# Optimization experiments

Hardware: AMD Instinct MI355X
Metric: run time of the kernel (lower is better)

## Reference

```python
import jax, jax.numpy as jnp
import numpy as np

N_NODES = 20000
N_EDGES = 640000
K_CHEB = 20


def setup_inputs() -> dict:
    key = jax.random.key(0)
    ks = jax.random.split(key, 8)
    x = jax.random.normal(ks[0], (128, N_NODES, 1), dtype=jnp.float32)
    rows = jax.random.randint(ks[1], (N_EDGES,), 0, N_NODES, dtype=jnp.int32)
    cols = jax.random.randint(ks[2], (N_EDGES,), 0, N_NODES, dtype=jnp.int32)
    # rescaled-Laplacian-like values, small scale so the K=20 recursion stays bounded
    vals = jax.random.normal(ks[3], (N_EDGES,), dtype=jnp.float32) * 0.05
    W_gc = jax.random.normal(ks[4], (K_CHEB, 10), dtype=jnp.float32) * 0.1
    b_gc = jnp.zeros((10,), dtype=jnp.float32)
    W_fc = jax.random.normal(ks[5], (N_NODES * 10, 10), dtype=jnp.float32) * 0.01
    b_fc = jnp.zeros((10,), dtype=jnp.float32)
    return {"x": x, "rows": rows, "cols": cols, "vals": vals,
            "W_gc": W_gc, "b_gc": b_gc, "W_fc": W_fc, "b_fc": b_fc}


def reference(x, rows, cols, vals, W_gc, b_gc, W_fc, b_fc):
    B, N, Fin = x.shape  # Fin == 1
    x0 = x[..., 0].T  # [N, B]

    def spmm(t):  # sparse L @ t via edge-list scatter-add, t: [N, B]
        return jax.ops.segment_sum(vals[:, None] * t[cols], rows, num_segments=N)

    # Chebyshev recursion: T0 = x, T1 = L x, Tk = 2 L T_{k-1} - T_{k-2}
    Ts = [x0, spmm(x0)]
    for _ in range(K_CHEB - 2):
        Ts.append(2.0 * spmm(Ts[-1]) - Ts[-2])
    Xt = jnp.stack(Ts, axis=-1)  # [N, B, K]

    gc = jnp.einsum('nbk,kf->bnf', Xt, W_gc) + b_gc  # [B, N, 10]
    gc = jax.nn.relu(gc)
    flat = gc.reshape(B, N * 10)
    h = jax.nn.relu(flat @ W_fc + b_fc)  # [B, 10]
    return jax.nn.softmax(h, axis=1)
```

## Files before the change

### kernel.cpp

```cpp
#include <hip/hip_runtime.h>
#include <hip/hip_bf16.h>
#include <hip/hip_fp16.h>
#include <math.h>


#define NF 10
#define KCHEB 20
#define BCG 64
#define COFF (KCHEB * BCG)

typedef unsigned int u32;


__global__ void init_kernel(int* counts, float* h_part, int N, int H) {
    int i = blockIdx.x * blockDim.x + threadIdx.x;
    if (i < N) counts[i] = 0;
    if (i < H) h_part[i] = 0.f;
}

__global__ void hist_kernel(const int* __restrict__ rows, int* __restrict__ counts, int E) {
    int e = blockIdx.x * blockDim.x + threadIdx.x;
    if (e < E) atomicAdd(&counts[rows[e]], 1);
}

#define SCAN_THREADS 1024
__global__ void scan_kernel(const int* __restrict__ counts, int* __restrict__ row_start,
                            int* __restrict__ cursor, int N) {
    __shared__ int sh[SCAN_THREADS];
    int t = threadIdx.x;
    int CH = (N + SCAN_THREADS - 1) / SCAN_THREADS;
    int base = t * CH;
    int sum = 0;
    for (int i = 0; i < CH; ++i) {
        int idx = base + i;
        sum += (idx < N) ? counts[idx] : 0;
    }
    sh[t] = sum;
    __syncthreads();
    for (int off = 1; off < SCAN_THREADS; off <<= 1) {
        int v = (t >= off) ? sh[t - off] : 0;
        __syncthreads();
        sh[t] += v;
        __syncthreads();
    }
    int run = (t == 0) ? 0 : sh[t - 1];
    for (int i = 0; i < CH; ++i) {
        int idx = base + i;
        if (idx < N) {
            int v = counts[idx];
            row_start[idx] = run;
            cursor[idx] = run;
            run += v;
        }
    }
    if (t == SCAN_THREADS - 1) row_start[N] = run;
}

__global__ void scatter_kernel(const int* __restrict__ rows, const int* __restrict__ cols,
                               const float* __restrict__ vals, int* __restrict__ cursor,
                               int2* __restrict__ csr, int E) {
    int e = blockIdx.x * blockDim.x + threadIdx.x;
    if (e >= E) return;
    int p = atomicAdd(&cursor[rows[e]], 1);
    csr[p] = make_int2(cols[e] * BCG, __float_as_int(vals[e]));
}


__global__ void transpose_kernel(const float* __restrict__ x, float* __restrict__ Xt32,
                                 __half* __restrict__ X16, int N, int ntiles, int b0s) {
    __shared__ float tile[BCG][65];
    int tid = threadIdx.x;
    int g = blockIdx.x / ntiles;
    int ti = blockIdx.x - g * ntiles;
    int n0 = ti * 64;
#pragma unroll
    for (int p = 0; p < 16; ++p) {
        int idx = p * 256 + tid;
        int row = idx >> 6;
        int col = idx & 63;
        if (n0 + col < N)
            tile[row][col] = x[(size_t)(b0s + g * BCG + row) * N + n0 + col];
    }
    __syncthreads();
#pragma unroll
    for (int p = 0; p < 16; ++p) {
        int idx = p * 256 + tid;
        int nloc = idx >> 6;
        int bb = idx & 63;
        int n = n0 + nloc;
        if (n < N) {
            float v = tile[bb][nloc];
            Xt32[((size_t)g * N + n) * COFF + bb] = v;
            X16[((size_t)(g * 2 + 0) * N + n) * BCG + bb] = __float2half_rn(v);
        }
    }
}


__global__ __launch_bounds__(256)
void spmm_kernel(float* __restrict__ Xt32, __half* __restrict__ X16,
                 const int* __restrict__ row_start, const int2* __restrict__ csr,
                 int N, int xpcShift, int subsPerChunk,
                 int ringIn, int ringOut, int kPrev, int kOut,
                 float alpha, float beta) {
    int xcd = blockIdx.x & 7;
    int chunk = xcd >> xpcShift;
    int xpcMask = (1 << xpcShift) - 1;
    int sub = (blockIdx.x >> 3) * (1 << xpcShift) + (xcd & xpcMask);
    if (sub >= subsPerChunk) return;
    int tid = threadIdx.x;
    int ln = tid >> 3;
    int bq = tid & 7;
    int n = sub * 32 + ln;
    if (n >= N) return;
    int s = row_start[n];
    int e = row_start[n + 1];

    const __half* gin = X16 + ((size_t)(chunk * 2 + ringIn) * N) * BCG;
    int bo = bq * 8;
    float acc[8];
#pragma unroll
    for (int q = 0; q < 8; ++q) acc[q] = 0.f;

    int i = s;
    for (; i + 4 <= e; i += 4) {
        int2 p0 = csr[i], p1 = csr[i + 1], p2 = csr[i + 2], p3 = csr[i + 3];
        uint4 u0 = *(const uint4*)(gin + p0.x + bo);
        uint4 u1 = *(const uint4*)(gin + p1.x + bo);
        uint4 u2 = *(const uint4*)(gin + p2.x + bo);
        uint4 u3 = *(const uint4*)(gin + p3.x + bo);
        float v0 = __int_as_float(p0.y), v1 = __int_as_float(p1.y);
        float v2 = __int_as_float(p2.y), v3 = __int_as_float(p3.y);
        {
            float2 f0 = __half22float2(*(__half2*)&u0.x), f1 = __half22float2(*(__half2*)&u0.y);
            float2 f2 = __half22float2(*(__half2*)&u0.z), f3 = __half22float2(*(__half2*)&u0.w);
            acc[0] += v0 * f0.x; acc[1] += v0 * f0.y; acc[2] += v0 * f1.x; acc[3] += v0 * f1.y;
            acc[4] += v0 * f2.x; acc[5] += v0 * f2.y; acc[6] += v0 * f3.x; acc[7] += v0 * f3.y;
        }
        {
            float2 f0 = __half22float2(*(__half2*)&u1.x), f1 = __half22float2(*(__half2*)&u1.y);
            float2 f2 = __half22float2(*(__half2*)&u1.z), f3 = __half22float2(*(__half2*)&u1.w);
            acc[0] += v1 * f0.x; acc[1] += v1 * f0.y; acc[2] += v1 * f1.x; acc[3] += v1 * f1.y;
            acc[4] += v1 * f2.x; acc[5] += v1 * f2.y; acc[6] += v1 * f3.x; acc[7] += v1 * f3.y;
        }
        {
            float2 f0 = __half22float2(*(__half2*)&u2.x), f1 = __half22float2(*(__half2*)&u2.y);
            float2 f2 = __half22float2(*(__half2*)&u2.z), f3 = __half22float2(*(__half2*)&u2.w);
            acc[0] += v2 * f0.x; acc[1] += v2 * f0.y; acc[2] += v2 * f1.x; acc[3] += v2 * f1.y;
            acc[4] += v2 * f2.x; acc[5] += v2 * f2.y; acc[6] += v2 * f3.x; acc[7] += v2 * f3.y;
        }
        {
            float2 f0 = __half22float2(*(__half2*)&u3.x), f1 = __half22float2(*(__half2*)&u3.y);
            float2 f2 = __half22float2(*(__half2*)&u3.z), f3 = __half22float2(*(__half2*)&u3.w);
            acc[0] += v3 * f0.x; acc[1] += v3 * f0.y; acc[2] += v3 * f1.x; acc[3] += v3 * f1.y;
            acc[4] += v3 * f2.x; acc[5] += v3 * f2.y; acc[6] += v3 * f3.x; acc[7] += v3 * f3.y;
        }
    }
    for (; i < e; ++i) {
        int2 p0 = csr[i];
        uint4 u0 = *(const uint4*)(gin + p0.x + bo);
        float v0 = __int_as_float(p0.y);
        float2 f0 = __half22float2(*(__half2*)&u0.x), f1 = __half22float2(*(__half2*)&u0.y);
        float2 f2 = __half22float2(*(__half2*)&u0.z), f3 = __half22float2(*(__half2*)&u0.w);
        acc[0] += v0 * f0.x; acc[1] += v0 * f0.y; acc[2] += v0 * f1.x; acc[3] += v0 * f1.y;
        acc[4] += v0 * f2.x; acc[5] += v0 * f2.y; acc[6] += v0 * f3.x; acc[7] += v0 * f3.y;
    }

    float* c32 = Xt32 + (size_t)chunk * N * COFF + (size_t)n * COFF;
    float o[8];
#pragma unroll
    for (int q = 0; q < 8; ++q) o[q] = alpha * acc[q];
    if (beta != 0.f) {
        const float4 pv0 = *(const float4*)(c32 + kPrev * BCG + bo);
        const float4 pv1 = *(const float4*)(c32 + kPrev * BCG + bo + 4);
        o[0] += beta * pv0.x; o[1] += beta * pv0.y; o[2] += beta * pv0.z; o[3] += beta * pv0.w;
        o[4] += beta * pv1.x; o[5] += beta * pv1.y; o[6] += beta * pv1.z; o[7] += beta * pv1.w;
    }
    *(float4*)(c32 + kOut * BCG + bo)     = make_float4(o[0], o[1], o[2], o[3]);
    *(float4*)(c32 + kOut * BCG + bo + 4) = make_float4(o[4], o[5], o[6], o[7]);
    __half* o16 = X16 + ((size_t)(chunk * 2 + ringOut) * N + n) * BCG + bo;
    uint4 h4;
    __half2 h01 = __floats2half2_rn(o[0], o[1]);
    __half2 h23 = __floats2half2_rn(o[2], o[3]);
    __half2 h45 = __floats2half2_rn(o[4], o[5]);
    __half2 h67 = __floats2half2_rn(o[6], o[7]);
    h4.x = *(u32*)&h01; h4.y = *(u32*)&h23; h4.z = *(u32*)&h45; h4.w = *(u32*)&h67;
    *(uint4*)o16 = h4;
}


__global__ __launch_bounds__(256, 4)
void proj_fc_kernel(const float* __restrict__ Xt32,
                    const float* __restrict__ W_gc,
                    const float* __restrict__ b_gc,
                    const float* __restrict__ W_fc,
                    float* __restrict__ h_part,
                    int N, int b0s, int G) {
    __shared__ float sWgT[NF * KCHEB];
    __shared__ float sbg[NF];
    __shared__ float sRed[BCG * 11];
    __shared__ float sWf[4 * NF * 12];
    int tid = threadIdx.x;
    if (tid < KCHEB * NF) sWgT[(tid % NF) * KCHEB + tid / NF] = W_gc[tid];
    if (tid < NF) sbg[tid] = b_gc[tid];
    for (int i = tid; i < BCG * 11; i += 256) sRed[i] = 0.f;
    __syncthreads();

    int g = blockIdx.x % G;
    int bidx = blockIdx.x / G;
    int nblk = gridDim.x / G;

    int bb = tid & (BCG - 1);
    int ln = tid >> 6;

    float h_loc[NF];
#pragma unroll
    for (int f = 0; f < NF; ++f) h_loc[f] = 0.f;

    const float* chunkBase = Xt32 + (size_t)g * N * COFF;
    int ngroups = (N + 3) / 4;
    for (int grp = bidx; grp < ngroups; grp += nblk) {
        int n0 = grp * 4;
        int lim = (N - n0 < 4 ? N - n0 : 4) * (NF * NF);
        int o = tid * 4;
        if (o < lim) {
            float4 w = *(const float4*)(W_fc + (size_t)n0 * (NF * NF) + o);
            int slot = o / 100;
            int rem = o - slot * 100;
            int j = rem / 10;
            int f = rem - j * 10;
            float wv[4] = { w.x, w.y, w.z, w.w };
#pragma unroll
            for (int q = 0; q < 4; ++q) {
                sWf[slot * 120 + j * 12 + f] = wv[q];
                if (++f == 10) { f = 0; if (++j == 10) { j = 0; ++slot; } }
            }
        }
        __syncthreads();

        int n = n0 + ln;
        if (n < N) {
            float xt[KCHEB];
            const float* xp = chunkBase + (size_t)n * COFF + bb;
#pragma unroll
            for (int k = 0; k < KCHEB; ++k) xt[k] = xp[k * BCG];
            const float* wrow = sWf + ln * 120;
#pragma unroll
            for (int j = 0; j < NF; ++j) {
                const float4 g0 = *(const float4*)(sWgT + j * KCHEB + 0);
                const float4 g1 = *(const float4*)(sWgT + j * KCHEB + 4);
                const float4 g2 = *(const float4*)(sWgT + j * KCHEB + 8);
                const float4 g3 = *(const float4*)(sWgT + j * KCHEB + 12);
                const float4 g4 = *(const float4*)(sWgT + j * KCHEB + 16);
                float gc = sbg[j]
                    + g0.x * xt[0]  + g0.y * xt[1]  + g0.z * xt[2]  + g0.w * xt[3]
                    + g1.x * xt[4]  + g1.y * xt[5]  + g1.z * xt[6]  + g1.w * xt[7]
                    + g2.x * xt[8]  + g2.y * xt[9]  + g2.z * xt[10] + g2.w * xt[11]
                    + g3.x * xt[12] + g3.y * xt[13] + g3.z * xt[14] + g3.w * xt[15]
                    + g4.x * xt[16] + g4.y * xt[17] + g4.z * xt[18] + g4.w * xt[19];
                gc = fmaxf(gc, 0.f);
                const float4 w0 = *(const float4*)(wrow + j * 12 + 0);
                const float4 w1 = *(const float4*)(wrow + j * 12 + 4);
                const float2 w2 = *(const float2*)(wrow + j * 12 + 8);
                h_loc[0] += gc * w0.x; h_loc[1] += gc * w0.y;
                h_loc[2] += gc * w0.z; h_loc[3] += gc * w0.w;
                h_loc[4] += gc * w1.x; h_loc[5] += gc * w1.y;
                h_loc[6] += gc * w1.z; h_loc[7] += gc * w1.w;
                h_loc[8] += gc * w2.x; h_loc[9] += gc * w2.y;
            }
        }
        __syncthreads();
    }
#pragma unroll
    for (int f = 0; f < NF; ++f) atomicAdd(&sRed[bb * 11 + f], h_loc[f]);
    __syncthreads();
    for (int i = tid; i < BCG * NF; i += 256) {
        int rb = i / NF;
        int rf = i - rb * NF;
        atomicAdd(&h_part[(size_t)(b0s + g * BCG + rb) * NF + rf], sRed[rb * 11 + rf]);
    }
}


__global__ void softmax_kernel(const float* __restrict__ h_part, const float* __restrict__ b_fc,
                               float* __restrict__ out, int B) {
    int b = blockIdx.x * blockDim.x + threadIdx.x;
    if (b >= B) return;
    float v[NF];
    float m = -1e30f;
#pragma unroll
    for (int f = 0; f < NF; ++f) {
        float t = fmaxf(h_part[b * NF + f] + b_fc[f], 0.f);
        v[f] = t;
        m = fmaxf(m, t);
    }
    float s = 0.f;
#pragma unroll
    for (int f = 0; f < NF; ++f) { v[f] = expf(v[f] - m); s += v[f]; }
    float inv = 1.f / s;
#pragma unroll
    for (int f = 0; f < NF; ++f) out[b * NF + f] = v[f] * inv;
}


extern "C" void kernel_launch(void* const* d_in, const int* in_sizes, int n_in,
                              void* d_out, int out_size, void* d_ws, size_t ws_size,
                              hipStream_t stream) {
    const float* x    = (const float*)d_in[0];
    const int*   rows = (const int*)d_in[1];
    const int*   cols = (const int*)d_in[2];
    const float* vals = (const float*)d_in[3];
    const float* W_gc = (const float*)d_in[4];
    const float* b_gc = (const float*)d_in[5];
    const float* W_fc = (const float*)d_in[6];
    const float* b_fc = (const float*)d_in[7];
    float* out = (float*)d_out;

    const int E = in_sizes[1];
    const int N = in_sizes[6] / (NF * NF);
    const int B = in_sizes[0] / N;

    char* p = (char*)d_ws;
    int* counts    = (int*)p;   p += sizeof(int) * (size_t)N;
    int* row_start = (int*)p;   p += sizeof(int) * (size_t)(N + 1);
    int* cursor    = (int*)p;   p += sizeof(int) * (size_t)N;
    p = (char*)(((size_t)p + 15) & ~(size_t)15);
    int2* csr      = (int2*)p;  p += sizeof(int2) * (size_t)E;
    float* h_part  = (float*)p; p += sizeof(float) * (size_t)B * NF;
    size_t fixed = (size_t)(p - (char*)d_ws);
    fixed = (fixed + 255) & ~(size_t)255;

    size_t perChunk32 = (size_t)N * COFF * sizeof(float);
    size_t perChunk16 = (size_t)2 * N * BCG * sizeof(__half);
    int G = (B >= 2 * BCG) ? 2 : 1;
    while (G > 1 && fixed + (size_t)G * (perChunk32 + perChunk16) > ws_size) G >>= 1;
    __half* X16 = (__half*)((char*)d_ws + fixed);
    size_t x16b = ((size_t)G * perChunk16 + 255) & ~(size_t)255;
    float* Xt32 = (float*)((char*)d_ws + fixed + x16b);
    int xpcShift = (G == 2) ? 2 : 3;
    int BT = G * BCG;
    int nsc = B / BT;

    {
        int H = B * NF;
        int cov = (N > H) ? N : H;
        init_kernel<<<(cov + 255) / 256, 256, 0, stream>>>(counts, h_part, N, H);
        hist_kernel<<<(E + 255) / 256, 256, 0, stream>>>(rows, counts, E);
        scan_kernel<<<1, SCAN_THREADS, 0, stream>>>(counts, row_start, cursor, N);
        scatter_kernel<<<(E + 255) / 256, 256, 0, stream>>>(rows, cols, vals, cursor, csr, E);
    }

    int ntiles = (N + 63) / 64;
    int subsPerChunk = (N + 31) / 32;
    int xpc = 1 << xpcShift;
    int gridSpmm = 8 * ((subsPerChunk + xpc - 1) / xpc);

    for (int c = 0; c < nsc; ++c) {
        int b0s = c * BT;
        transpose_kernel<<<G * ntiles, 256, 0, stream>>>(x, Xt32, X16, N, ntiles, b0s);
        for (int k = 1; k < KCHEB; ++k) {
            float alpha = (k == 1) ? 1.f : 2.f;
            float beta  = (k == 1) ? 0.f : -1.f;
            spmm_kernel<<<gridSpmm, 256, 0, stream>>>(
                Xt32, X16, row_start, csr, N, xpcShift, subsPerChunk,
                (k - 1) & 1, k & 1, (k >= 2) ? (k - 2) : 0, k, alpha, beta);
        }
        proj_fc_kernel<<<512 * G, 256, 0, stream>>>(Xt32, W_gc, b_gc, W_fc, h_part, N, b0s, G);
    }

    softmax_kernel<<<1, 128, 0, stream>>>(h_part, b_fc, out, B);
}
```

Baseline: 605.0 us.

## Store full Chebyshev history in fp16 and keep only a two-slot fp32 carry

The full K-term Chebyshev history moves from an fp32 array into an fp16 array indexed per node with stride K*64. A small two-slot fp32 ring carries T_{k-2}/T_{k-1} for the recurrence. The projection kernel now reads half-precision history, which halves its read traffic and the workspace size. In exchange, SpMM gathers now use a stride of K*64 halves per node instead of a dense 64-wide ring, which may hurt cache locality, and the projection consumes fp16-rounded values.

```diff
diff --git a/kernel.cpp b/kernel.cpp
--- a/kernel.cpp
+++ b/kernel.cpp
@@ -7,7 +7,7 @@
 #define NF 10
 #define KCHEB 20
 #define BCG 64
-#define COFF (KCHEB * BCG)
+#define COFF16 (KCHEB * BCG)
 
 typedef unsigned int u32;
 
@@ -62,12 +62,12 @@
     int e = blockIdx.x * blockDim.x + threadIdx.x;
     if (e >= E) return;
     int p = atomicAdd(&cursor[rows[e]], 1);
-    csr[p] = make_int2(cols[e] * BCG, __float_as_int(vals[e]));
-}
-
-
-__global__ void transpose_kernel(const float* __restrict__ x, float* __restrict__ Xt32,
-                                 __half* __restrict__ X16, int N, int ntiles, int b0s) {
+    csr[p] = make_int2(cols[e] * COFF16, __float_as_int(vals[e]));
+}
+
+
+__global__ void transpose_kernel(const float* __restrict__ x, __half* __restrict__ X16,
+                                 float* __restrict__ C32, int N, int ntiles, int b0s) {
     __shared__ float tile[BCG][65];
     int tid = threadIdx.x;
     int g = blockIdx.x / ntiles;
@@ -90,19 +90,18 @@
         int n = n0 + nloc;
         if (n < N) {
             float v = tile[bb][nloc];
-            Xt32[((size_t)g * N + n) * COFF + bb] = v;
-            X16[((size_t)(g * 2 + 0) * N + n) * BCG + bb] = __float2half_rn(v);
+            X16[(size_t)(g * N + n) * COFF16 + bb] = __float2half_rn(v);
+            C32[((size_t)(g * 2 + 0) * N + n) * BCG + bb] = v;
         }
     }
 }
 
 
 __global__ __launch_bounds__(256)
-void spmm_kernel(float* __restrict__ Xt32, __half* __restrict__ X16,
+void spmm_kernel(__half* __restrict__ X16, float* __restrict__ C32,
                  const int* __restrict__ row_start, const int2* __restrict__ csr,
                  int N, int xpcShift, int subsPerChunk,
-                 int ringIn, int ringOut, int kPrev, int kOut,
-                 float alpha, float beta) {
+                 int kIn, int kOut, float alpha, float beta) {
     int xcd = blockIdx.x & 7;
     int chunk = xcd >> xpcShift;
     int xpcMask = (1 << xpcShift) - 1;
@@ -116,7 +115,8 @@
     int s = row_start[n];
     int e = row_start[n + 1];
 
-    const __half* gin = X16 + ((size_t)(chunk * 2 + ringIn) * N) * BCG;
+    const __half* gin = X16 + (size_t)chunk * N * COFF16;
+    int koff = kIn * BCG + bq * 8;
     int bo = bq * 8;
     float acc[8];
 #pragma unroll
@@ -125,10 +125,10 @@
     int i = s;
     for (; i + 4 <= e; i += 4) {
         int2 p0 = csr[i], p1 = csr[i + 1], p2 = csr[i + 2], p3 = csr[i + 3];
-        uint4 u0 = *(const uint4*)(gin + p0.x + bo);
-        uint4 u1 = *(const uint4*)(gin + p1.x + bo);
-        uint4 u2 = *(const uint4*)(gin + p2.x + bo);
-        uint4 u3 = *(const uint4*)(gin + p3.x + bo);
+        uint4 u0 = *(const uint4*)(gin + p0.x + koff);
+        uint4 u1 = *(const uint4*)(gin + p1.x + koff);
+        uint4 u2 = *(const uint4*)(gin + p2.x + koff);
+        uint4 u3 = *(const uint4*)(gin + p3.x + koff);
         float v0 = __int_as_float(p0.y), v1 = __int_as_float(p1.y);
         float v2 = __int_as_float(p2.y), v3 = __int_as_float(p3.y);
         {
@@ -158,7 +158,7 @@
     }
     for (; i < e; ++i) {
         int2 p0 = csr[i];
-        uint4 u0 = *(const uint4*)(gin + p0.x + bo);
+        uint4 u0 = *(const uint4*)(gin + p0.x + koff);
         float v0 = __int_as_float(p0.y);
         float2 f0 = __half22float2(*(__half2*)&u0.x), f1 = __half22float2(*(__half2*)&u0.y);
         float2 f2 = __half22float2(*(__half2*)&u0.z), f3 = __half22float2(*(__half2*)&u0.w);
@@ -166,19 +166,19 @@
         acc[4] += v0 * f2.x; acc[5] += v0 * f2.y; acc[6] += v0 * f3.x; acc[7] += v0 * f3.y;
     }
 
-    float* c32 = Xt32 + (size_t)chunk * N * COFF + (size_t)n * COFF;
+    float* cslot = C32 + ((size_t)(chunk * 2 + (kOut & 1)) * N + n) * BCG + bo;
     float o[8];
 #pragma unroll
     for (int q = 0; q < 8; ++q) o[q] = alpha * acc[q];
     if (beta != 0.f) {
-        const float4 pv0 = *(const float4*)(c32 + kPrev * BCG + bo);
-        const float4 pv1 = *(const float4*)(c32 + kPrev * BCG + bo + 4);
+        const float4 pv0 = *(const float4*)(cslot);
+        const float4 pv1 = *(const float4*)(cslot + 4);
         o[0] += beta * pv0.x; o[1] += beta * pv0.y; o[2] += beta * pv0.z; o[3] += beta * pv0.w;
         o[4] += beta * pv1.x; o[5] += beta * pv1.y; o[6] += beta * pv1.z; o[7] += beta * pv1.w;
     }
-    *(float4*)(c32 + kOut * BCG + bo)     = make_float4(o[0], o[1], o[2], o[3]);
-    *(float4*)(c32 + kOut * BCG + bo + 4) = make_float4(o[4], o[5], o[6], o[7]);
-    __half* o16 = X16 + ((size_t)(chunk * 2 + ringOut) * N + n) * BCG + bo;
+    *(float4*)(cslot)     = make_float4(o[0], o[1], o[2], o[3]);
+    *(float4*)(cslot + 4) = make_float4(o[4], o[5], o[6], o[7]);
+    __half* o16 = X16 + (size_t)(chunk * N + n) * COFF16 + kOut * BCG + bo;
     uint4 h4;
     __half2 h01 = __floats2half2_rn(o[0], o[1]);
     __half2 h23 = __floats2half2_rn(o[2], o[3]);
@@ -190,7 +190,7 @@
 
 
 __global__ __launch_bounds__(256, 4)
-void proj_fc_kernel(const float* __restrict__ Xt32,
+void proj_fc_kernel(const __half* __restrict__ X16,
                     const float* __restrict__ W_gc,
                     const float* __restrict__ b_gc,
                     const float* __restrict__ W_fc,
@@ -217,7 +217,7 @@
 #pragma unroll
     for (int f = 0; f < NF; ++f) h_loc[f] = 0.f;
 
-    const float* chunkBase = Xt32 + (size_t)g * N * COFF;
+    const __half* chunkBase = X16 + (size_t)g * N * COFF16;
     int ngroups = (N + 3) / 4;
     for (int grp = bidx; grp < ngroups; grp += nblk) {
         int n0 = grp * 4;
@@ -241,9 +241,9 @@
         int n = n0 + ln;
         if (n < N) {
             float xt[KCHEB];
-            const float* xp = chunkBase + (size_t)n * COFF + bb;
-#pragma unroll
-            for (int k = 0; k < KCHEB; ++k) xt[k] = xp[k * BCG];
+            const __half* xp = chunkBase + (size_t)n * COFF16 + bb;
+#pragma unroll
+            for (int k = 0; k < KCHEB; ++k) xt[k] = __half2float(xp[k * BCG]);
             const float* wrow = sWf + ln * 120;
 #pragma unroll
             for (int j = 0; j < NF; ++j) {
@@ -330,13 +330,13 @@
     size_t fixed = (size_t)(p - (char*)d_ws);
     fixed = (fixed + 255) & ~(size_t)255;
 
-    size_t perChunk32 = (size_t)N * COFF * sizeof(float);
-    size_t perChunk16 = (size_t)2 * N * BCG * sizeof(__half);
+    size_t perChunk16 = (size_t)N * COFF16 * sizeof(__half);
+    size_t perCarry   = (size_t)2 * N * BCG * sizeof(float);
     int G = (B >= 2 * BCG) ? 2 : 1;
-    while (G > 1 && fixed + (size_t)G * (perChunk32 + perChunk16) > ws_size) G >>= 1;
+    while (G > 1 && fixed + (size_t)G * (perChunk16 + perCarry) > ws_size) G >>= 1;
     __half* X16 = (__half*)((char*)d_ws + fixed);
     size_t x16b = ((size_t)G * perChunk16 + 255) & ~(size_t)255;
-    float* Xt32 = (float*)((char*)d_ws + fixed + x16b);
+    float* C32 = (float*)((char*)d_ws + fixed + x16b);
     int xpcShift = (G == 2) ? 2 : 3;
     int BT = G * BCG;
     int nsc = B / BT;
@@ -357,15 +357,15 @@
 
     for (int c = 0; c < nsc; ++c) {
         int b0s = c * BT;
-        transpose_kernel<<<G * ntiles, 256, 0, stream>>>(x, Xt32, X16, N, ntiles, b0s);
+        transpose_kernel<<<G * ntiles, 256, 0, stream>>>(x, X16, C32, N, ntiles, b0s);
         for (int k = 1; k < KCHEB; ++k) {
             float alpha = (k == 1) ? 1.f : 2.f;
             float beta  = (k == 1) ? 0.f : -1.f;
             spmm_kernel<<<gridSpmm, 256, 0, stream>>>(
-                Xt32, X16, row_start, csr, N, xpcShift, subsPerChunk,
-                (k - 1) & 1, k & 1, (k >= 2) ? (k - 2) : 0, k, alpha, beta);
-        }
-        proj_fc_kernel<<<512 * G, 256, 0, stream>>>(Xt32, W_gc, b_gc, W_fc, h_part, N, b0s, G);
+                X16, C32, row_start, csr, N, xpcShift, subsPerChunk,
+                k - 1, k, alpha, beta);
+        }
+        proj_fc_kernel<<<512 * G, 256, 0, stream>>>(X16, W_gc, b_gc, W_fc, h_part, N, b0s, G);
     }
 
     softmax_kernel<<<1, 128, 0, stream>>>(h_part, b_fc, out, B);
```

New measurement: 596.2 us (median of 2 runs). About the same (-1.5%).
